# Optimization experiments

Hardware: AMD Instinct MI355X
Metric: run time of the kernel (lower is better)

The kernel has to match this reference:

```python
import jax, jax.numpy as jnp
import numpy as np

B, S, E, D, OUT = 128, 128, 256, 256, 64


def setup_inputs() -> dict:
    key = jax.random.key(0)
    ks = jax.random.split(key, 10)
    w = lambda k, shp, s=0.05: (jax.random.normal(k, shp, dtype=jnp.float32) * s)
    return {
        "input_encoded": jax.random.normal(ks[0], (B, S, E), dtype=jnp.float32),
        "y_history": jax.random.normal(ks[1], (B, S, OUT), dtype=jnp.float32),
        "h0": jax.random.normal(ks[2], (B, D), dtype=jnp.float32) * 0.1,
        "c0": jax.random.normal(ks[3], (B, D), dtype=jnp.float32) * 0.1,
        "attn_W1": w(ks[4], (2 * D + E, E)),
        "attn_b1": jnp.zeros((E,), jnp.float32),
        "attn_w2": w(ks[5], (E,)),
        "attn_b2": jnp.zeros((1,), jnp.float32),
        "lstm_Wih": w(ks[6], (OUT, 4 * D)),
        "lstm_Whh": w(ks[7], (D, 4 * D)),
        "lstm_bih": jnp.zeros((4 * D,), jnp.float32),
        "lstm_bhh": jnp.zeros((4 * D,), jnp.float32),
        "fc_W": w(ks[8], (E + OUT, OUT)),
        "fc_b": jnp.zeros((OUT,), jnp.float32),
        "fc_out_W": w(ks[9], (D + E, OUT * S)),
        "fc_out_b": jnp.zeros((OUT * S,), jnp.float32),
    }


def reference(input_encoded, y_history, h0, c0, attn_W1, attn_b1, attn_w2, attn_b2,
              lstm_Wih, lstm_Whh, lstm_bih, lstm_bhh, fc_W, fc_b, fc_out_W, fc_out_b):
    # Split the attn first-layer weight according to the concat order (h, c, enc).
    Wh, Wc, We = attn_W1[:D], attn_W1[D:2 * D], attn_W1[2 * D:]
    # Encoder projection is time-invariant across decoder steps; hoist it.
    enc_proj = jnp.einsum('bse,ef->bsf', input_encoded, We)  # [B,S,E]

    def step(carry, y_t):
        h, c, _ = carry
        hc = h @ Wh + c @ Wc + attn_b1                       # [B,E]
        pre = jnp.tanh(enc_proj + hc[:, None, :])            # [B,S,E]
        scores = pre @ attn_w2 + attn_b2[0]                  # [B,S]
        alpha = jax.nn.softmax(scores, axis=1)
        context = jnp.einsum('bs,bse->be', alpha, input_encoded)  # [B,E]
        y_tilde = jnp.concatenate([context, y_t], axis=1) @ fc_W + fc_b  # [B,OUT]
        gates = y_tilde @ lstm_Wih + lstm_bih + h @ lstm_Whh + lstm_bhh  # [B,4D]
        i, f, g, o = jnp.split(gates, 4, axis=1)  # pytorch gate order i,f,g,o
        c_new = jax.nn.sigmoid(f) * c + jax.nn.sigmoid(i) * jnp.tanh(g)
        h_new = jax.nn.sigmoid(o) * jnp.tanh(c_new)
        return (h_new, c_new, context), None

    y_seq = jnp.transpose(y_history, (1, 0, 2))  # [S,B,OUT]
    (h_T, c_T, context_T), _ = jax.lax.scan(step, (h0, c0, jnp.zeros((B, E), h0.dtype)), y_seq)
    out = jnp.concatenate([h_T, context_T], axis=1) @ fc_out_W + fc_out_b  # [B,OUT*S]
    return out.reshape(-1, S, OUT)
```

## Files before the change

kernel.cpp:

```cpp
#include <hip/hip_runtime.h>

#define BB 128
#define SS 128
#define EE 256
#define DD 256
#define OO 64

#define W1_OFF   0
#define WHH_OFF  196608
#define WIH_OFF  458752
#define FCW_OFF  524288
#define WTOTAL   544768

__device__ __forceinline__ float fsig(float x) { return 1.0f / (1.0f + __expf(-x)); }
__device__ __forceinline__ float ftanh(float x) {
    float t = __expf(-2.0f * fabsf(x));
    float r = (1.0f - t) / (1.0f + t);
    return copysignf(r, x);
}
__device__ __forceinline__ int SWZ(int e) { return (e & ~31) | ((e + 4 * (e >> 5)) & 31); }

__device__ __forceinline__ void fma8(const uint4 w, const float xv, float* acc) {
    acc[0] += xv * __uint_as_float(w.x << 16);
    acc[1] += xv * __uint_as_float(w.x & 0xffff0000u);
    acc[2] += xv * __uint_as_float(w.y << 16);
    acc[3] += xv * __uint_as_float(w.y & 0xffff0000u);
    acc[4] += xv * __uint_as_float(w.z << 16);
    acc[5] += xv * __uint_as_float(w.z & 0xffff0000u);
    acc[6] += xv * __uint_as_float(w.w << 16);
    acc[7] += xv * __uint_as_float(w.w & 0xffff0000u);
}

__global__ __launch_bounds__(256) void conv_kernel(
    const float* __restrict__ W1, const float* __restrict__ Whh,
    const float* __restrict__ Wih, const float* __restrict__ fcW,
    unsigned short* __restrict__ out)
{
    const int idx = blockIdx.x * 256 + threadIdx.x;
    float f;
    if      (idx < WHH_OFF)  f = W1[idx];
    else if (idx < WIH_OFF)  f = Whh[idx - WHH_OFF];
    else if (idx < FCW_OFF)  f = Wih[idx - WIH_OFF];
    else if (idx < WTOTAL)   f = fcW[idx - FCW_OFF];
    else return;
    unsigned int u = __float_as_uint(f);
    u = (u + 0x7fffu + ((u >> 16) & 1u)) >> 16;
    out[idx] = (unsigned short)u;
}

__global__ __launch_bounds__(1024, 4) void scan_kernel(
    const float* __restrict__ inp,
    const float* __restrict__ yhist,
    const float* __restrict__ h0, const float* __restrict__ c0,
    const float* __restrict__ W1f,
    const float* __restrict__ b1, const float* __restrict__ w2, const float* __restrict__ b2,
    const float* __restrict__ bih, const float* __restrict__ bhh,
    const float* __restrict__ fcb,
    const unsigned short* __restrict__ wbf,
    float* __restrict__ hctxT)
{
    __shared__ float sh_h[DD], sh_c[DD], sh_hc[EE];
    __shared__ float sh_gh[1024];
    __shared__ float sh_w2[EE];
    __shared__ float sh_b1[EE], sh_bs[1024];
    __shared__ float sh_raw[SS];
    __shared__ float sh_ctx[EE], sh_y[OO], sh_yt[OO], sh_fcb[OO];
    __shared__ float sh_misc[1];
    __shared__ float red1[32 * 256];
    __shared__ float red2[8 * 1024];

    const int b = blockIdx.x, t = threadIdx.x;
    const float* inp_b = inp + b * SS * EE;
    const unsigned short* W1bf  = wbf + W1_OFF;
    const unsigned short* Whhbf = wbf + WHH_OFF;
    const unsigned short* Wihbf = wbf + WIH_OFF;
    const unsigned short* fcWbf = wbf + FCW_OFF;
    const float b2v = b2[0];

    const int e8  = (t & 31) * 8,  kc1 = t >> 5;
    const int j8  = (t & 127) * 8, kc2 = t >> 7;
    const int s_own = t >> 3,      a2  = t & 7, e0 = a2 * 32;
    const int e4  = (t & 63) * 4,  sc  = t >> 6;
    const int o4  = (t & 15) * 4,  kc3 = t >> 4;

    if (t < 256) {
        sh_h[t] = h0[b * 256 + t]; sh_c[t] = c0[b * 256 + t];
        sh_b1[t] = b1[t];
        sh_w2[SWZ(t)] = w2[t];
    }
    if (t < 64) sh_fcb[t] = fcb[t];
    sh_bs[t] = bih[t] + bhh[t];

    float er[32];
    #pragma unroll
    for (int j = 0; j < 32; ++j) er[j] = 0.f;
    {
        const float* We = W1f + 512 * 256;
        for (int kc = 0; kc < 16; ++kc) {
            {
                const int row = t >> 6, c4 = (t & 63) * 4;
                float4 v = *(const float4*)(We + (size_t)(kc * 16 + row) * 256 + c4);
                *(float4*)&red1[row * 256 + c4] = v;
            }
            {
                const int s = t >> 3, k2 = (t & 7) * 2;
                float2 v = *(const float2*)(inp_b + s * 256 + kc * 16 + k2);
                red1[4096 + s * 16 + k2] = v.x;
                red1[4096 + s * 16 + k2 + 1] = v.y;
            }
            __syncthreads();
            for (int k = 0; k < 16; ++k) {
                const float xv = red1[4096 + s_own * 16 + k];
                #pragma unroll
                for (int j4 = 0; j4 < 8; ++j4) {
                    float4 w = *(const float4*)&red1[k * 256 + e0 + j4 * 4];
                    er[j4*4+0] += xv * w.x; er[j4*4+1] += xv * w.y;
                    er[j4*4+2] += xv * w.z; er[j4*4+3] += xv * w.w;
                }
            }
            __syncthreads();
        }
    }

    for (int ts = 0; ts < SS; ++ts) {
        if (t < 64) sh_y[t] = yhist[b * SS * OO + ts * OO + t];

        {
            float acc[8];
            #pragma unroll
            for (int r = 0; r < 8; ++r) acc[r] = 0.f;
            #pragma unroll 4
            for (int k = kc1 * 16; k < kc1 * 16 + 16; ++k) {
                const float xv = (k < 256) ? sh_h[k] : sh_c[k - 256];
                uint4 w = *(const uint4*)(W1bf + (size_t)k * 256 + e8);
                fma8(w, xv, acc);
            }
            *(float4*)&red1[kc1 * 256 + e8]     = make_float4(acc[0], acc[1], acc[2], acc[3]);
            *(float4*)&red1[kc1 * 256 + e8 + 4] = make_float4(acc[4], acc[5], acc[6], acc[7]);
        }
        {
            float acc[8];
            #pragma unroll
            for (int r = 0; r < 8; ++r) acc[r] = 0.f;
            #pragma unroll 4
            for (int k = kc2 * 32; k < kc2 * 32 + 32; ++k) {
                const float hv = sh_h[k];
                uint4 w = *(const uint4*)(Whhbf + (size_t)k * 1024 + j8);
                fma8(w, hv, acc);
            }
            *(float4*)&red2[kc2 * 1024 + j8]     = make_float4(acc[0], acc[1], acc[2], acc[3]);
            *(float4*)&red2[kc2 * 1024 + j8 + 4] = make_float4(acc[4], acc[5], acc[6], acc[7]);
        }
        __syncthreads();
        if (t < 256) {
            float v = sh_b1[t];
            #pragma unroll 8
            for (int kc = 0; kc < 32; ++kc) v += red1[kc * 256 + t];
            sh_hc[SWZ(t)] = v;
        }
        {
            float v = 0.f;
            #pragma unroll
            for (int kc = 0; kc < 8; ++kc) v += red2[kc * 1024 + t];
            sh_gh[t] = v;
        }
        __syncthreads();

        {
            float acc = 0.f;
            #pragma unroll
            for (int j4 = 0; j4 < 8; ++j4) {
                const int phys = e0 + ((j4 * 4 + 4 * a2) & 31);
                float4 hc4 = *(const float4*)&sh_hc[phys];
                float4 w24 = *(const float4*)&sh_w2[phys];
                acc += ftanh(er[j4*4+0] + hc4.x) * w24.x;
                acc += ftanh(er[j4*4+1] + hc4.y) * w24.y;
                acc += ftanh(er[j4*4+2] + hc4.z) * w24.z;
                acc += ftanh(er[j4*4+3] + hc4.w) * w24.w;
            }
            acc += __shfl_xor(acc, 1);
            acc += __shfl_xor(acc, 2);
            acc += __shfl_xor(acc, 4);
            if (a2 == 0) sh_raw[s_own] = __expf(acc + b2v);
        }
        __syncthreads();
        if (t < 64) {
            float v = sh_raw[t] + sh_raw[t + 64];
            #pragma unroll
            for (int m = 32; m > 0; m >>= 1) v += __shfl_xor(v, m);
            if (t == 0) sh_misc[0] = 1.0f / v;
        }
        __syncthreads();

        {
            float ax = 0.f, ay = 0.f, az = 0.f, aw = 0.f;
            for (int s = sc * 8; s < sc * 8 + 8; ++s) {
                const float al = sh_raw[s];
                float4 iv = *(const float4*)(inp_b + s * 256 + e4);
                ax += al * iv.x; ay += al * iv.y; az += al * iv.z; aw += al * iv.w;
            }
            *(float4*)&red1[sc * 256 + e4] = make_float4(ax, ay, az, aw);
        }
        __syncthreads();
        if (t < 256) {
            float v = 0.f;
            #pragma unroll
            for (int k = 0; k < 16; ++k) v += red1[k * 256 + t];
            v *= sh_misc[0];
            sh_ctx[t] = v;
            if (ts == SS - 1) hctxT[(size_t)(256 + t) * 128 + b] = v;
        }
        __syncthreads();

        {
            float acc[4] = {0.f, 0.f, 0.f, 0.f};
            for (int kk = kc3 * 5; kk < kc3 * 5 + 5; ++kk) {
                const float val = (kk < 256) ? sh_ctx[kk] : sh_y[kk - 256];
                uint2 w = *(const uint2*)(fcWbf + kk * 64 + o4);
                acc[0] += val * __uint_as_float(w.x << 16);
                acc[1] += val * __uint_as_float(w.x & 0xffff0000u);
                acc[2] += val * __uint_as_float(w.y << 16);
                acc[3] += val * __uint_as_float(w.y & 0xffff0000u);
            }
            *(float4*)&red1[kc3 * 64 + o4] = make_float4(acc[0], acc[1], acc[2], acc[3]);
        }
        __syncthreads();
        if (t < 64) {
            float v = sh_fcb[t];
            #pragma unroll 16
            for (int kc = 0; kc < 64; ++kc) v += red1[kc * 64 + t];
            sh_yt[t] = v;
        }
        __syncthreads();

        {
            float acc[8];
            #pragma unroll
            for (int r = 0; r < 8; ++r) acc[r] = 0.f;
            #pragma unroll
            for (int k = kc2 * 8; k < kc2 * 8 + 8; ++k) {
                const float yv = sh_yt[k];
                uint4 w = *(const uint4*)(Wihbf + (size_t)k * 1024 + j8);
                fma8(w, yv, acc);
            }
            *(float4*)&red2[kc2 * 1024 + j8]     = make_float4(acc[0], acc[1], acc[2], acc[3]);
            *(float4*)&red2[kc2 * 1024 + j8 + 4] = make_float4(acc[4], acc[5], acc[6], acc[7]);
        }
        __syncthreads();
        {
            float v = sh_gh[t] + sh_bs[t];
            #pragma unroll
            for (int kc = 0; kc < 8; ++kc) v += red2[kc * 1024 + t];
            red1[t] = v;
        }
        __syncthreads();
        if (t < 256) {
            const float gi = red1[t], gf = red1[256 + t], gg = red1[512 + t], go = red1[768 + t];
            const float cn = fsig(gf) * sh_c[t] + fsig(gi) * ftanh(gg);
            sh_c[t] = cn;
            const float hn = fsig(go) * ftanh(cn);
            sh_h[t] = hn;
            if (ts == SS - 1) hctxT[(size_t)t * 128 + b] = hn;
        }
        __syncthreads();
    }
}

__global__ __launch_bounds__(256) void out_gemm(
    const float* __restrict__ AT, const float* __restrict__ W,
    const float* __restrict__ bias, float* __restrict__ out)
{
    __shared__ float Ab[64 * 132];
    __shared__ float Bb[64 * 32];
    const int t = threadIdx.x;
    const int nt = blockIdx.x * 32;
    const int n4 = (t & 7) * 4;
    const int m4 = (t >> 3) * 4;
    float acc[4][4];
    #pragma unroll
    for (int i = 0; i < 4; ++i)
        #pragma unroll
        for (int jj = 0; jj < 4; ++jj) acc[i][jj] = 0.f;

    for (int kc = 0; kc < 8; ++kc) {
        #pragma unroll
        for (int i = 0; i < 8; ++i) {
            const int flat4 = i * 256 + t;
            const int row = flat4 >> 5, mm4 = (flat4 & 31) * 4;
            float4 v = *(const float4*)(AT + (size_t)(kc * 64 + row) * 128 + mm4);
            *(float4*)&Ab[row * 132 + mm4] = v;
        }
        #pragma unroll
        for (int i = 0; i < 2; ++i) {
            const int fl = t + i * 256;
            const int k = fl >> 3, nn4 = (fl & 7) * 4;
            *(float4*)&Bb[k * 32 + nn4] =
                *(const float4*)(W + (size_t)(kc * 64 + k) * 8192 + nt + nn4);
        }
        __syncthreads();
        for (int k = 0; k < 64; ++k) {
            const float4 bv = *(const float4*)&Bb[k * 32 + n4];
            const float4 av = *(const float4*)&Ab[k * 132 + m4];
            acc[0][0] += av.x * bv.x; acc[0][1] += av.x * bv.y; acc[0][2] += av.x * bv.z; acc[0][3] += av.x * bv.w;
            acc[1][0] += av.y * bv.x; acc[1][1] += av.y * bv.y; acc[1][2] += av.y * bv.z; acc[1][3] += av.y * bv.w;
            acc[2][0] += av.z * bv.x; acc[2][1] += av.z * bv.y; acc[2][2] += av.z * bv.z; acc[2][3] += av.z * bv.w;
            acc[3][0] += av.w * bv.x; acc[3][1] += av.w * bv.y; acc[3][2] += av.w * bv.z; acc[3][3] += av.w * bv.w;
        }
        __syncthreads();
    }
    const float4 bb = *(const float4*)(bias + nt + n4);
    #pragma unroll
    for (int i = 0; i < 4; ++i) {
        float4 r;
        r.x = acc[i][0] + bb.x; r.y = acc[i][1] + bb.y;
        r.z = acc[i][2] + bb.z; r.w = acc[i][3] + bb.w;
        *(float4*)(out + (size_t)(m4 + i) * 8192 + nt + n4) = r;
    }
}

extern "C" void kernel_launch(void* const* d_in, const int* in_sizes, int n_in,
                              void* d_out, int out_size, void* d_ws, size_t ws_size,
                              hipStream_t stream) {
    const float* inp = (const float*)d_in[0];
    const float* yh  = (const float*)d_in[1];
    const float* h0  = (const float*)d_in[2];
    const float* c0  = (const float*)d_in[3];
    const float* W1  = (const float*)d_in[4];
    const float* b1  = (const float*)d_in[5];
    const float* w2  = (const float*)d_in[6];
    const float* b2  = (const float*)d_in[7];
    const float* Wih = (const float*)d_in[8];
    const float* Whh = (const float*)d_in[9];
    const float* bih = (const float*)d_in[10];
    const float* bhh = (const float*)d_in[11];
    const float* fcW = (const float*)d_in[12];
    const float* fcb = (const float*)d_in[13];
    const float* foW = (const float*)d_in[14];
    const float* fob = (const float*)d_in[15];

    float* hctxT = (float*)d_ws;
    unsigned short* wbf = (unsigned short*)d_out;

    conv_kernel<<<dim3((WTOTAL + 255) / 256), dim3(256), 0, stream>>>(W1, Whh, Wih, fcW, wbf);
    scan_kernel<<<dim3(BB), dim3(1024), 0, stream>>>(
        inp, yh, h0, c0, W1, b1, w2, b2, bih, bhh, fcb, wbf, hctxT);
    out_gemm<<<dim3(8192 / 32), dim3(256), 0, stream>>>(hctxT, foW, fob, (float*)d_out);
}
```

Before: 4.855 ms.

## Cache encoder input in LDS and replace staged reductions with LDS atomics

Loads the block's whole input_encoded slice (128 KB) into shared memory once, so the attention context pass reads LDS instead of global memory every step. The two-phase partial-sum reductions (write partials, sync, sum) are replaced by shared-memory atomicAdd into zeroed accumulators. This removes several __syncthreads per timestep and shrinks the reduction buffers. The Whh gate accumulators are also kept in registers across the step and folded into the Wih accumulation. Atomic contention on LDS and the much larger shared footprint, which limits blocks per CU, may offset the saved barriers.

```diff
diff --git a/kernel.cpp b/kernel.cpp
--- a/kernel.cpp
+++ b/kernel.cpp
@@ -12,6 +12,11 @@
 #define FCW_OFF  524288
 #define WTOTAL   544768
 
+#define GB  0
+#define HCB 1024
+#define CXB 1280
+#define YTB 1536
+
 __device__ __forceinline__ float fsig(float x) { return 1.0f / (1.0f + __expf(-x)); }
 __device__ __forceinline__ float ftanh(float x) {
     float t = __expf(-2.0f * fabsf(x));
@@ -19,16 +24,14 @@
     return copysignf(r, x);
 }
 __device__ __forceinline__ int SWZ(int e) { return (e & ~31) | ((e + 4 * (e >> 5)) & 31); }
+__device__ __forceinline__ float bflo(unsigned int u) { return __uint_as_float(u << 16); }
+__device__ __forceinline__ float bfhi(unsigned int u) { return __uint_as_float(u & 0xffff0000u); }
 
 __device__ __forceinline__ void fma8(const uint4 w, const float xv, float* acc) {
-    acc[0] += xv * __uint_as_float(w.x << 16);
-    acc[1] += xv * __uint_as_float(w.x & 0xffff0000u);
-    acc[2] += xv * __uint_as_float(w.y << 16);
-    acc[3] += xv * __uint_as_float(w.y & 0xffff0000u);
-    acc[4] += xv * __uint_as_float(w.z << 16);
-    acc[5] += xv * __uint_as_float(w.z & 0xffff0000u);
-    acc[6] += xv * __uint_as_float(w.w << 16);
-    acc[7] += xv * __uint_as_float(w.w & 0xffff0000u);
+    acc[0] += xv * bflo(w.x); acc[1] += xv * bfhi(w.x);
+    acc[2] += xv * bflo(w.y); acc[3] += xv * bfhi(w.y);
+    acc[4] += xv * bflo(w.z); acc[5] += xv * bfhi(w.z);
+    acc[6] += xv * bflo(w.w); acc[7] += xv * bfhi(w.w);
 }
 
 __global__ __launch_bounds__(256) void conv_kernel(
@@ -59,18 +62,18 @@
     const unsigned short* __restrict__ wbf,
     float* __restrict__ hctxT)
 {
-    __shared__ float sh_h[DD], sh_c[DD], sh_hc[EE];
-    __shared__ float sh_gh[1024];
+    __shared__ float sh_inp[SS * EE];
+    __shared__ float red[4096];
+    __shared__ float sh_h[DD], sh_c[DD];
     __shared__ float sh_w2[EE];
-    __shared__ float sh_b1[EE], sh_bs[1024];
+    __shared__ float sh_b1[EE];
+    __shared__ float sh_bs[1024];
     __shared__ float sh_raw[SS];
-    __shared__ float sh_ctx[EE], sh_y[OO], sh_yt[OO], sh_fcb[OO];
+    __shared__ float sh_y[OO], sh_fcb[OO];
     __shared__ float sh_misc[1];
-    __shared__ float red1[32 * 256];
-    __shared__ float red2[8 * 1024];
 
     const int b = blockIdx.x, t = threadIdx.x;
-    const float* inp_b = inp + b * SS * EE;
+    const float* inp_b = inp + (size_t)b * SS * EE;
     const unsigned short* W1bf  = wbf + W1_OFF;
     const unsigned short* Whhbf = wbf + WHH_OFF;
     const unsigned short* Wihbf = wbf + WIH_OFF;
@@ -83,6 +86,12 @@
     const int e4  = (t & 63) * 4,  sc  = t >> 6;
     const int o4  = (t & 15) * 4,  kc3 = t >> 4;
 
+    #pragma unroll
+    for (int i = 0; i < 8; ++i) {
+        const int idx = i * 1024 + t;
+        const int s = idx >> 6, c4 = (idx & 63) * 4;
+        *(float4*)&sh_inp[s * 256 + c4] = *(const float4*)(inp_b + (size_t)idx * 4);
+    }
     if (t < 256) {
         sh_h[t] = h0[b * 256 + t]; sh_c[t] = c0[b * 256 + t];
         sh_b1[t] = b1[t];
@@ -90,6 +99,7 @@
     }
     if (t < 64) sh_fcb[t] = fcb[t];
     sh_bs[t] = bih[t] + bhh[t];
+    __syncthreads();
 
     float er[32];
     #pragma unroll
@@ -99,31 +109,34 @@
         for (int kc = 0; kc < 16; ++kc) {
             {
                 const int row = t >> 6, c4 = (t & 63) * 4;
-                float4 v = *(const float4*)(We + (size_t)(kc * 16 + row) * 256 + c4);
-                *(float4*)&red1[row * 256 + c4] = v;
-            }
-            {
-                const int s = t >> 3, k2 = (t & 7) * 2;
-                float2 v = *(const float2*)(inp_b + s * 256 + kc * 16 + k2);
-                red1[4096 + s * 16 + k2] = v.x;
-                red1[4096 + s * 16 + k2 + 1] = v.y;
+                *(float4*)&red[row * 256 + c4] =
+                    *(const float4*)(We + (size_t)(kc * 16 + row) * 256 + c4);
             }
             __syncthreads();
             for (int k = 0; k < 16; ++k) {
-                const float xv = red1[4096 + s_own * 16 + k];
+                const float xv = sh_inp[s_own * 256 + kc * 16 + k];
                 #pragma unroll
                 for (int j4 = 0; j4 < 8; ++j4) {
-                    float4 w = *(const float4*)&red1[k * 256 + e0 + j4 * 4];
+                    float4 w = *(const float4*)&red[k * 256 + e0 + j4 * 4];
                     er[j4*4+0] += xv * w.x; er[j4*4+1] += xv * w.y;
                     er[j4*4+2] += xv * w.z; er[j4*4+3] += xv * w.w;
                 }
             }
             __syncthreads();
         }
-    }
+        #pragma unroll
+        for (int j4 = 0; j4 < 8; ++j4) {
+            float4 v = *(const float4*)&sh_b1[e0 + j4 * 4];
+            er[j4*4+0] += v.x; er[j4*4+1] += v.y; er[j4*4+2] += v.z; er[j4*4+3] += v.w;
+        }
+    }
+    red[t] = 0.f;
+    if (t < 256) { red[HCB + t] = 0.f; red[CXB + t] = 0.f; }
+    if (t < 64)  red[YTB + t] = 0.f;
+    __syncthreads();
 
     for (int ts = 0; ts < SS; ++ts) {
-        if (t < 64) sh_y[t] = yhist[b * SS * OO + ts * OO + t];
+        if (t < 64) sh_y[t] = yhist[(size_t)b * SS * OO + ts * OO + t];
 
         {
             float acc[8];
@@ -135,34 +148,17 @@
                 uint4 w = *(const uint4*)(W1bf + (size_t)k * 256 + e8);
                 fma8(w, xv, acc);
             }
-            *(float4*)&red1[kc1 * 256 + e8]     = make_float4(acc[0], acc[1], acc[2], acc[3]);
-            *(float4*)&red1[kc1 * 256 + e8 + 4] = make_float4(acc[4], acc[5], acc[6], acc[7]);
-        }
-        {
-            float acc[8];
-            #pragma unroll
-            for (int r = 0; r < 8; ++r) acc[r] = 0.f;
-            #pragma unroll 4
-            for (int k = kc2 * 32; k < kc2 * 32 + 32; ++k) {
-                const float hv = sh_h[k];
-                uint4 w = *(const uint4*)(Whhbf + (size_t)k * 1024 + j8);
-                fma8(w, hv, acc);
-            }
-            *(float4*)&red2[kc2 * 1024 + j8]     = make_float4(acc[0], acc[1], acc[2], acc[3]);
-            *(float4*)&red2[kc2 * 1024 + j8 + 4] = make_float4(acc[4], acc[5], acc[6], acc[7]);
-        }
-        __syncthreads();
-        if (t < 256) {
-            float v = sh_b1[t];
-            #pragma unroll 8
-            for (int kc = 0; kc < 32; ++kc) v += red1[kc * 256 + t];
-            sh_hc[SWZ(t)] = v;
-        }
-        {
-            float v = 0.f;
-            #pragma unroll
-            for (int kc = 0; kc < 8; ++kc) v += red2[kc * 1024 + t];
-            sh_gh[t] = v;
+            #pragma unroll
+            for (int r = 0; r < 8; ++r) atomicAdd(&red[HCB + SWZ(e8 + r)], acc[r]);
+        }
+        float g[8];
+        #pragma unroll
+        for (int r = 0; r < 8; ++r) g[r] = (kc2 == 0) ? sh_bs[j8 + r] : 0.f;
+        #pragma unroll 8
+        for (int k = kc2 * 32; k < kc2 * 32 + 32; ++k) {
+            const float hv = sh_h[k];
+            uint4 w = *(const uint4*)(Whhbf + (size_t)k * 1024 + j8);
+            fma8(w, hv, g);
         }
         __syncthreads();
 
@@ -171,7 +167,7 @@
             #pragma unroll
             for (int j4 = 0; j4 < 8; ++j4) {
                 const int phys = e0 + ((j4 * 4 + 4 * a2) & 31);
-                float4 hc4 = *(const float4*)&sh_hc[phys];
+                float4 hc4 = *(const float4*)&red[HCB + phys];
                 float4 w24 = *(const float4*)&sh_w2[phys];
                 acc += ftanh(er[j4*4+0] + hc4.x) * w24.x;
                 acc += ftanh(er[j4*4+1] + hc4.y) * w24.y;
@@ -184,83 +180,75 @@
             if (a2 == 0) sh_raw[s_own] = __expf(acc + b2v);
         }
         __syncthreads();
+
         if (t < 64) {
             float v = sh_raw[t] + sh_raw[t + 64];
             #pragma unroll
             for (int m = 32; m > 0; m >>= 1) v += __shfl_xor(v, m);
             if (t == 0) sh_misc[0] = 1.0f / v;
         }
-        __syncthreads();
-
         {
             float ax = 0.f, ay = 0.f, az = 0.f, aw = 0.f;
-            for (int s = sc * 8; s < sc * 8 + 8; ++s) {
+            #pragma unroll
+            for (int i = 0; i < 8; ++i) {
+                const int s = sc * 8 + i;
                 const float al = sh_raw[s];
-                float4 iv = *(const float4*)(inp_b + s * 256 + e4);
+                float4 iv = *(const float4*)&sh_inp[s * 256 + e4];
                 ax += al * iv.x; ay += al * iv.y; az += al * iv.z; aw += al * iv.w;
             }
-            *(float4*)&red1[sc * 256 + e4] = make_float4(ax, ay, az, aw);
-        }
-        __syncthreads();
+            atomicAdd(&red[CXB + e4],     ax);
+            atomicAdd(&red[CXB + e4 + 1], ay);
+            atomicAdd(&red[CXB + e4 + 2], az);
+            atomicAdd(&red[CXB + e4 + 3], aw);
+        }
+        __syncthreads();
+
+        {
+            const float inv = sh_misc[0];
+            float acc[4];
+            #pragma unroll
+            for (int i = 0; i < 4; ++i) acc[i] = (kc3 == 0) ? sh_fcb[o4 + i] : 0.f;
+            #pragma unroll
+            for (int kk = kc3 * 5; kk < kc3 * 5 + 5; ++kk) {
+                const float val = (kk < 256) ? red[CXB + kk] * inv : sh_y[kk - 256];
+                uint2 w = *(const uint2*)(fcWbf + kk * 64 + o4);
+                acc[0] += val * bflo(w.x);
+                acc[1] += val * bfhi(w.x);
+                acc[2] += val * bflo(w.y);
+                acc[3] += val * bfhi(w.y);
+            }
+            #pragma unroll
+            for (int i = 0; i < 4; ++i) atomicAdd(&red[YTB + o4 + i], acc[i]);
+        }
+        __syncthreads();
+
+        {
+            #pragma unroll
+            for (int k = kc2 * 8; k < kc2 * 8 + 8; ++k) {
+                const float yv = red[YTB + k];
+                uint4 w = *(const uint4*)(Wihbf + (size_t)k * 1024 + j8);
+                fma8(w, yv, g);
+            }
+            #pragma unroll
+            for (int r = 0; r < 8; ++r) atomicAdd(&red[GB + j8 + r], g[r]);
+        }
+        __syncthreads();
+
         if (t < 256) {
-            float v = 0.f;
-            #pragma unroll
-            for (int k = 0; k < 16; ++k) v += red1[k * 256 + t];
-            v *= sh_misc[0];
-            sh_ctx[t] = v;
-            if (ts == SS - 1) hctxT[(size_t)(256 + t) * 128 + b] = v;
-        }
-        __syncthreads();
-
-        {
-            float acc[4] = {0.f, 0.f, 0.f, 0.f};
-            for (int kk = kc3 * 5; kk < kc3 * 5 + 5; ++kk) {
-                const float val = (kk < 256) ? sh_ctx[kk] : sh_y[kk - 256];
-                uint2 w = *(const uint2*)(fcWbf + kk * 64 + o4);
-                acc[0] += val * __uint_as_float(w.x << 16);
-                acc[1] += val * __uint_as_float(w.x & 0xffff0000u);
-                acc[2] += val * __uint_as_float(w.y << 16);
-                acc[3] += val * __uint_as_float(w.y & 0xffff0000u);
-            }
-            *(float4*)&red1[kc3 * 64 + o4] = make_float4(acc[0], acc[1], acc[2], acc[3]);
-        }
-        __syncthreads();
-        if (t < 64) {
-            float v = sh_fcb[t];
-            #pragma unroll 16
-            for (int kc = 0; kc < 64; ++kc) v += red1[kc * 64 + t];
-            sh_yt[t] = v;
-        }
-        __syncthreads();
-
-        {
-            float acc[8];
-            #pragma unroll
-            for (int r = 0; r < 8; ++r) acc[r] = 0.f;
-            #pragma unroll
-            for (int k = kc2 * 8; k < kc2 * 8 + 8; ++k) {
-                const float yv = sh_yt[k];
-                uint4 w = *(const uint4*)(Wihbf + (size_t)k * 1024 + j8);
-                fma8(w, yv, acc);
-            }
-            *(float4*)&red2[kc2 * 1024 + j8]     = make_float4(acc[0], acc[1], acc[2], acc[3]);
-            *(float4*)&red2[kc2 * 1024 + j8 + 4] = make_float4(acc[4], acc[5], acc[6], acc[7]);
-        }
-        __syncthreads();
-        {
-            float v = sh_gh[t] + sh_bs[t];
-            #pragma unroll
-            for (int kc = 0; kc < 8; ++kc) v += red2[kc * 1024 + t];
-            red1[t] = v;
-        }
-        __syncthreads();
-        if (t < 256) {
-            const float gi = red1[t], gf = red1[256 + t], gg = red1[512 + t], go = red1[768 + t];
+            const float gi = red[GB + t],       gf = red[GB + 256 + t];
+            const float gg = red[GB + 512 + t], go = red[GB + 768 + t];
             const float cn = fsig(gf) * sh_c[t] + fsig(gi) * ftanh(gg);
             sh_c[t] = cn;
             const float hn = fsig(go) * ftanh(cn);
             sh_h[t] = hn;
-            if (ts == SS - 1) hctxT[(size_t)t * 128 + b] = hn;
+            if (ts == SS - 1) {
+                hctxT[(size_t)t * 128 + b] = hn;
+                hctxT[(size_t)(256 + t) * 128 + b] = red[CXB + t] * sh_misc[0];
+            }
+            red[GB + t] = 0.f; red[GB + 256 + t] = 0.f;
+            red[GB + 512 + t] = 0.f; red[GB + 768 + t] = 0.f;
+            red[HCB + t] = 0.f; red[CXB + t] = 0.f;
+            if (t < 64) red[YTB + t] = 0.f;
         }
         __syncthreads();
     }
```

Result: slower. 8.563 ms (+76.4%).
